# Performance work log

Hardware: AMD Instinct MI355X
Metric: run time of the kernel (lower is better)

The kernel has to match this reference:

```python
import jax, jax.numpy as jnp
import numpy as np

B, S, D_IN, D_OUT, BLK = 2, 2048, 4096, 16384, 32
NBLK = D_IN // BLK  # 128


def setup_inputs() -> dict:
    key = jax.random.key(0)
    k_x, k_q, k_s, k_b = jax.random.split(key, 4)
    x = jax.random.normal(k_x, (B, S, D_IN), dtype=jnp.float32)
    # GGML Q8_0: signed 8-bit quants per block of 32
    qs = jax.random.randint(k_q, (D_OUT, NBLK, BLK), -128, 128, dtype=jnp.int32)
    # per-block scales (stand-in for the fp16 'd' field); small magnitude
    scales = jax.random.uniform(k_s, (D_OUT, NBLK), dtype=jnp.float32) * 0.02
    bias = jax.random.normal(k_b, (D_OUT,), dtype=jnp.float32)
    return {"x": x, "qs": qs, "scales": scales, "bias": bias}


def reference(x, qs, scales, bias):
    # _materialize_weight: block dequantize (d * q per block) then cast to input dtype
    # qs: [O, NBLK, BLK], scales: [O, NBLK] -> W: [O, D_IN]
    W = (scales[:, :, None] * qs.astype(x.dtype)).reshape(D_OUT, D_IN)
    # host Linear: y = x @ W^T + b
    y = jnp.einsum('bsd,od->bso', x, W) + bias
    return y
```

## Files before the change

kernel.cpp:

```cpp
#include <hip/hip_runtime.h>
#include <cstdint>
#include <cstddef>

#define M_DIM 4096
#define N_DIM 16384
#define K_DIM 4096
#define NBLK_Q 128

#define BM 256
#define BN 256
#define BK 64
#define KSTEPS (K_DIM / BK)
#define BUFB 32768
#define NBUF 2

typedef int i32x4 __attribute__((ext_vector_type(4)));
typedef int i32x16 __attribute__((ext_vector_type(16)));

#define SFENCE() __builtin_amdgcn_sched_barrier(0)

__global__ __launch_bounds__(256) void quant_x(const float* __restrict__ x,
                                               char* __restrict__ A8S,
                                               float* __restrict__ sxr) {
  const int m = blockIdx.x;
  const int t = threadIdx.x;
  const float* xr = x + (size_t)m * K_DIM + t * 16;
  float4 v[4];
#pragma unroll
  for (int i = 0; i < 4; ++i) v[i] = ((const float4*)xr)[i];
  float amax = 0.f;
#pragma unroll
  for (int i = 0; i < 4; ++i)
    amax = fmaxf(amax, fmaxf(fmaxf(fabsf(v[i].x), fabsf(v[i].y)),
                             fmaxf(fabsf(v[i].z), fabsf(v[i].w))));
#pragma unroll
  for (int off = 32; off; off >>= 1) amax = fmaxf(amax, __shfl_xor(amax, off, 64));
  __shared__ float wmax[4];
  if ((t & 63) == 0) wmax[t >> 6] = amax;
  __syncthreads();
  amax = fmaxf(fmaxf(wmax[0], wmax[1]), fmaxf(wmax[2], wmax[3]));
  const float inv = 127.0f / amax;
  if (t == 0) sxr[m] = amax / 127.0f;
  unsigned d[4];
#pragma unroll
  for (int i = 0; i < 4; ++i) {
    int q0 = (int)rintf(v[i].x * inv), q1 = (int)rintf(v[i].y * inv);
    int q2 = (int)rintf(v[i].z * inv), q3 = (int)rintf(v[i].w * inv);
    d[i] = (q0 & 0xff) | ((q1 & 0xff) << 8) | ((q2 & 0xff) << 16) | ((q3 & 0xff) << 24);
  }
  const int k32 = t >> 1, kg = t & 1;
  const int mtile = m >> 8, mm = m & 255, m32 = mm >> 5, r = mm & 31;
  int4* dst = (int4*)(A8S + ((size_t)(mtile * 128 + k32)) * 8192 + m32 * 1024 + kg * 512 + r * 16);
  *dst = make_int4(d[0], d[1], d[2], d[3]);
}

__global__ __launch_bounds__(256) void pack_w8(const int* __restrict__ qs,
                                               const float* __restrict__ scales,
                                               char* __restrict__ B8S,
                                               float* __restrict__ swc) {
  const int o = blockIdx.x * 4 + (threadIdx.x >> 6);
  const int l = threadIdx.x & 63;
  const float s0 = scales[(size_t)o * NBLK_Q + l];
  const float s1 = scales[(size_t)o * NBLK_Q + 64 + l];
  float S = fmaxf(s0, s1);
#pragma unroll
  for (int off = 32; off; off >>= 1) S = fmaxf(S, __shfl_xor(S, off, 64));
  if (l == 0) swc[o] = S;
  const float rS = 1.0f / S;
  const int nt = o >> 8, col = o & 255, n32 = col >> 5, c = col & 31;
#pragma unroll
  for (int h = 0; h < 2; ++h) {
    const int nb = l + 64 * h;
    const float ratio = ((h == 0) ? s0 : s1) * rS;
    const int4* q = (const int4*)(qs + ((size_t)o * NBLK_Q + nb) * 32);
    unsigned d[8];
#pragma unroll
    for (int g = 0; g < 8; ++g) {
      int4 v = q[g];
      int a0 = (int)rintf((float)v.x * ratio);
      int a1 = (int)rintf((float)v.y * ratio);
      int a2 = (int)rintf((float)v.z * ratio);
      int a3 = (int)rintf((float)v.w * ratio);
      d[g] = (a0 & 0xff) | ((a1 & 0xff) << 8) | ((a2 & 0xff) << 16) | ((a3 & 0xff) << 24);
    }
    char* dst = B8S + ((size_t)(nt * 128 + nb)) * 8192 + n32 * 1024 + c * 16;
    ((int4*)dst)[0] = make_int4(d[0], d[1], d[2], d[3]);
    ((int4*)(dst + 512))[0] = make_int4(d[4], d[5], d[6], d[7]);
  }
}

__global__ __launch_bounds__(512, 2) void gemm_i8(
    const char* __restrict__ A8S, const char* __restrict__ B8S,
    const float* __restrict__ sxr, const float* __restrict__ swc,
    const float* __restrict__ bias, float* __restrict__ C) {
  __shared__ __align__(16) char lds[NBUF * BUFB];

  const int tid = threadIdx.x;
  const int w = tid >> 6;
  const int l = tid & 63;
  const int wm = w >> 2;
  const int wn = w & 3;

  const int bid = blockIdx.x;
  const int xcd = bid & 7;
  const int k = bid >> 3;
  const int mtile = xcd * 2 + (k & 1);
  const int ntile = k >> 1;
  const int brow = mtile * BM;
  const int bcol = ntile * BN;

  const char* srcA = A8S + (size_t)mtile * 128 * 8192 + w * 1024 + l * 16;
  const char* srcB = B8S + (size_t)ntile * 128 * 8192 + w * 1024 + l * 16;
  const int doff = w * 1024 + l * 16;

  i32x16 acc[4][2] = {};

  {
    int4 ra0 = *(const int4*)(srcA);
    int4 ra1 = *(const int4*)(srcA + 8192);
    int4 rb0 = *(const int4*)(srcB);
    int4 rb1 = *(const int4*)(srcB + 8192);
    *(int4*)(lds + doff) = ra0;
    *(int4*)(lds + 16384 + doff) = ra1;
    *(int4*)(lds + 8192 + doff) = rb0;
    *(int4*)(lds + 24576 + doff) = rb1;
    __syncthreads();
  }

  for (int kt = 0; kt < KSTEPS; ++kt) {
    const char* bb = lds + (kt & 1) * BUFB;

    i32x4 a[2][4], b[2][2];
#pragma unroll
    for (int s = 0; s < 2; ++s) {
#pragma unroll
      for (int i = 0; i < 4; ++i)
        a[s][i] = *(const i32x4*)(bb + s * 16384 + (wm * 4 + i) * 1024 + l * 16);
#pragma unroll
      for (int j = 0; j < 2; ++j)
        b[s][j] = *(const i32x4*)(bb + s * 16384 + 8192 + (wn * 2 + j) * 1024 + l * 16);
    }

    const int qn = (kt + 1 > KSTEPS - 1) ? (KSTEPS - 1) : (kt + 1);
    const size_t go = (size_t)qn * 16384;
    int4 ra0 = *(const int4*)(srcA + go);
    int4 ra1 = *(const int4*)(srcA + go + 8192);
    int4 rb0 = *(const int4*)(srcB + go);
    int4 rb1 = *(const int4*)(srcB + go + 8192);

    SFENCE();
    __builtin_amdgcn_s_setprio(1);
#pragma unroll
    for (int i = 0; i < 4; ++i)
#pragma unroll
      for (int j = 0; j < 2; ++j) {
        acc[i][j] = __builtin_amdgcn_mfma_i32_32x32x32_i8(a[0][i], b[0][j], acc[i][j], 0, 0, 0);
        acc[i][j] = __builtin_amdgcn_mfma_i32_32x32x32_i8(a[1][i], b[1][j], acc[i][j], 0, 0, 0);
      }
    __builtin_amdgcn_s_setprio(0);
    SFENCE();

    char* nb = lds + ((kt + 1) & 1) * BUFB;
    *(int4*)(nb + doff) = ra0;
    *(int4*)(nb + 16384 + doff) = ra1;
    *(int4*)(nb + 8192 + doff) = rb0;
    *(int4*)(nb + 24576 + doff) = rb1;
    __syncthreads();
  }

#pragma unroll
  for (int i = 0; i < 4; ++i) {
    const int rb = brow + wm * 128 + i * 32 + 4 * (l >> 5);
#pragma unroll
    for (int j = 0; j < 2; ++j) {
      const int col = bcol + wn * 64 + j * 32 + (l & 31);
      const float Sw = swc[col];
      const float bv = bias[col];
#pragma unroll
      for (int r = 0; r < 16; ++r) {
        const int row = rb + (r & 3) + 8 * (r >> 2);
        C[(size_t)row * N_DIM + col] = (float)acc[i][j][r] * (sxr[row] * Sw) + bv;
      }
    }
  }
}

__global__ void naive_gemm(const float* __restrict__ x, const int* __restrict__ qs,
                           const float* __restrict__ scales, const float* __restrict__ bias,
                           float* __restrict__ y) {
  size_t idx = (size_t)blockIdx.x * 256 + threadIdx.x;
  if (idx >= (size_t)M_DIM * N_DIM) return;
  int o = (int)(idx % N_DIM);
  size_t m = idx / N_DIM;
  const float* xr = x + m * K_DIM;
  const int* q = qs + (size_t)o * K_DIM;
  const float* sc = scales + (size_t)o * NBLK_Q;
  float sum = 0.f;
  for (int nb = 0; nb < NBLK_Q; ++nb) {
    float s = sc[nb];
    float bs = 0.f;
#pragma unroll 8
    for (int b = 0; b < 32; ++b) bs += xr[nb * 32 + b] * (float)q[nb * 32 + b];
    sum += s * bs;
  }
  y[idx] = sum + bias[o];
}

extern "C" void kernel_launch(void* const* d_in, const int* in_sizes, int n_in,
                              void* d_out, int out_size, void* d_ws, size_t ws_size,
                              hipStream_t stream) {
  const float* x = (const float*)d_in[0];
  const int* qs = (const int*)d_in[1];
  const float* scales = (const float*)d_in[2];
  const float* bias = (const float*)d_in[3];
  float* y = (float*)d_out;

  const size_t A8_bytes = (size_t)M_DIM * K_DIM;
  const size_t B8_bytes = (size_t)N_DIM * K_DIM;
  const size_t SX_bytes = (size_t)M_DIM * 4;
  const size_t SW_bytes = (size_t)N_DIM * 4;

  if (ws_size < A8_bytes + B8_bytes + SX_bytes + SW_bytes) {
    size_t total = (size_t)M_DIM * N_DIM;
    naive_gemm<<<(unsigned)((total + 255) / 256), 256, 0, stream>>>(x, qs, scales, bias, y);
    return;
  }

  char* A8S = (char*)d_ws;
  char* B8S = A8S + A8_bytes;
  float* sxr = (float*)(B8S + B8_bytes);
  float* swc = (float*)((char*)sxr + SX_bytes);

  quant_x<<<M_DIM, 256, 0, stream>>>(x, A8S, sxr);
  pack_w8<<<N_DIM / 4, 256, 0, stream>>>(qs, scales, B8S, swc);
  gemm_i8<<<(M_DIM / BM) * (N_DIM / BN), 512, 0, stream>>>(A8S, B8S, sxr, swc, bias, y);
}
```

Before: 455.3 us.

## Deepen int8 GEMM pipeline to four LDS buffers with register double-buffering

```diff
diff --git a/kernel.cpp b/kernel.cpp
--- a/kernel.cpp
+++ b/kernel.cpp
@@ -9,15 +9,18 @@
 
 #define BM 256
 #define BN 256
-#define BK 64
+#define BK 32
 #define KSTEPS (K_DIM / BK)
-#define BUFB 32768
-#define NBUF 2
+#define BUFB 16384
+#define NBUF 4
 
 typedef int i32x4 __attribute__((ext_vector_type(4)));
 typedef int i32x16 __attribute__((ext_vector_type(16)));
 
 #define SFENCE() __builtin_amdgcn_sched_barrier(0)
+#define BAR() __builtin_amdgcn_s_barrier()
+#define WAITVM(n) asm volatile("s_waitcnt vmcnt(" #n ")")
+#define WAITLG0() asm volatile("s_waitcnt lgkmcnt(0)")
 
 __global__ __launch_bounds__(256) void quant_x(const float* __restrict__ x,
                                                char* __restrict__ A8S,
@@ -111,62 +114,78 @@
 
   const char* srcA = A8S + (size_t)mtile * 128 * 8192 + w * 1024 + l * 16;
   const char* srcB = B8S + (size_t)ntile * 128 * 8192 + w * 1024 + l * 16;
-  const int doff = w * 1024 + l * 16;
+  const int doffA = w * 1024 + l * 16;
+  const int doffB = 8192 + w * 1024 + l * 16;
+  const int roffA = wm * 4096 + l * 16;
+  const int roffB = 8192 + wn * 2048 + l * 16;
 
   i32x16 acc[4][2] = {};
+  i32x4 a0[4], b0[2], a1[4], b1[2];
+  int4 gA0, gB0, gA1, gB1;
 
   {
-    int4 ra0 = *(const int4*)(srcA);
-    int4 ra1 = *(const int4*)(srcA + 8192);
-    int4 rb0 = *(const int4*)(srcB);
-    int4 rb1 = *(const int4*)(srcB + 8192);
-    *(int4*)(lds + doff) = ra0;
-    *(int4*)(lds + 16384 + doff) = ra1;
-    *(int4*)(lds + 8192 + doff) = rb0;
-    *(int4*)(lds + 24576 + doff) = rb1;
-    __syncthreads();
-  }
-
-  for (int kt = 0; kt < KSTEPS; ++kt) {
-    const char* bb = lds + (kt & 1) * BUFB;
-
-    i32x4 a[2][4], b[2][2];
-#pragma unroll
-    for (int s = 0; s < 2; ++s) {
-#pragma unroll
-      for (int i = 0; i < 4; ++i)
-        a[s][i] = *(const i32x4*)(bb + s * 16384 + (wm * 4 + i) * 1024 + l * 16);
-#pragma unroll
-      for (int j = 0; j < 2; ++j)
-        b[s][j] = *(const i32x4*)(bb + s * 16384 + 8192 + (wn * 2 + j) * 1024 + l * 16);
-    }
-
-    const int qn = (kt + 1 > KSTEPS - 1) ? (KSTEPS - 1) : (kt + 1);
-    const size_t go = (size_t)qn * 16384;
-    int4 ra0 = *(const int4*)(srcA + go);
-    int4 ra1 = *(const int4*)(srcA + go + 8192);
-    int4 rb0 = *(const int4*)(srcB + go);
-    int4 rb1 = *(const int4*)(srcB + go + 8192);
-
-    SFENCE();
-    __builtin_amdgcn_s_setprio(1);
+    int4 ta0 = *(const int4*)(srcA);
+    int4 tb0 = *(const int4*)(srcB);
+    int4 ta1 = *(const int4*)(srcA + 8192);
+    int4 tb1 = *(const int4*)(srcB + 8192);
+    *(int4*)(lds + doffA) = ta0;
+    *(int4*)(lds + doffB) = tb0;
+    *(int4*)(lds + BUFB + doffA) = ta1;
+    *(int4*)(lds + BUFB + doffB) = tb1;
+    gA0 = *(const int4*)(srcA + 2 * 8192);
+    gB0 = *(const int4*)(srcB + 2 * 8192);
+    WAITLG0();
+    SFENCE(); BAR(); SFENCE();
 #pragma unroll
     for (int i = 0; i < 4; ++i)
-#pragma unroll
-      for (int j = 0; j < 2; ++j) {
-        acc[i][j] = __builtin_amdgcn_mfma_i32_32x32x32_i8(a[0][i], b[0][j], acc[i][j], 0, 0, 0);
-        acc[i][j] = __builtin_amdgcn_mfma_i32_32x32x32_i8(a[1][i], b[1][j], acc[i][j], 0, 0, 0);
-      }
-    __builtin_amdgcn_s_setprio(0);
-    SFENCE();
-
-    char* nb = lds + ((kt + 1) & 1) * BUFB;
-    *(int4*)(nb + doff) = ra0;
-    *(int4*)(nb + 16384 + doff) = ra1;
-    *(int4*)(nb + 8192 + doff) = rb0;
-    *(int4*)(nb + 24576 + doff) = rb1;
-    __syncthreads();
-  }
+      a0[i] = *(const i32x4*)(lds + roffA + i * 1024);
+#pragma unroll
+    for (int j = 0; j < 2; ++j)
+      b0[j] = *(const i32x4*)(lds + roffB + j * 1024);
+  }
+
+#define STEP(KT, CA, CB, NA, NB, WA, WB, LA, LB)                               \
+  do {                                                                         \
+    const char* rb = lds + (((KT) + 1) & 3) * BUFB;                            \
+    NA[0] = *(const i32x4*)(rb + roffA);                                       \
+    NA[1] = *(const i32x4*)(rb + roffA + 1024);                                \
+    NA[2] = *(const i32x4*)(rb + roffA + 2048);                                \
+    NA[3] = *(const i32x4*)(rb + roffA + 3072);                                \
+    NB[0] = *(const i32x4*)(rb + roffB);                                       \
+    NB[1] = *(const i32x4*)(rb + roffB + 1024);                                \
+    {                                                                          \
+      const int ql = ((KT) + 3 > KSTEPS - 1) ? (KSTEPS - 1) : ((KT) + 3);      \
+      LA = *(const int4*)(srcA + (size_t)ql * 8192);                           \
+      LB = *(const int4*)(srcB + (size_t)ql * 8192);                           \
+    }                                                                          \
+    SFENCE();                                                                  \
+    __builtin_amdgcn_s_setprio(1);                                             \
+    acc[0][0] = __builtin_amdgcn_mfma_i32_32x32x32_i8(CA[0], CB[0], acc[0][0], 0, 0, 0); \
+    acc[0][1] = __builtin_amdgcn_mfma_i32_32x32x32_i8(CA[0], CB[1], acc[0][1], 0, 0, 0); \
+    acc[1][0] = __builtin_amdgcn_mfma_i32_32x32x32_i8(CA[1], CB[0], acc[1][0], 0, 0, 0); \
+    acc[1][1] = __builtin_amdgcn_mfma_i32_32x32x32_i8(CA[1], CB[1], acc[1][1], 0, 0, 0); \
+    acc[2][0] = __builtin_amdgcn_mfma_i32_32x32x32_i8(CA[2], CB[0], acc[2][0], 0, 0, 0); \
+    acc[2][1] = __builtin_amdgcn_mfma_i32_32x32x32_i8(CA[2], CB[1], acc[2][1], 0, 0, 0); \
+    acc[3][0] = __builtin_amdgcn_mfma_i32_32x32x32_i8(CA[3], CB[0], acc[3][0], 0, 0, 0); \
+    acc[3][1] = __builtin_amdgcn_mfma_i32_32x32x32_i8(CA[3], CB[1], acc[3][1], 0, 0, 0); \
+    __builtin_amdgcn_s_setprio(0);                                             \
+    SFENCE();                                                                  \
+    WAITVM(2);                                                                 \
+    {                                                                          \
+      char* wb = lds + (((KT) + 2) & 3) * BUFB;                                \
+      *(int4*)(wb + doffA) = WA;                                               \
+      *(int4*)(wb + doffB) = WB;                                               \
+    }                                                                          \
+    SFENCE();                                                                  \
+    WAITLG0();                                                                 \
+    SFENCE(); BAR(); SFENCE();                                                 \
+  } while (0)
+
+  for (int kt = 0; kt < KSTEPS; kt += 2) {
+    STEP(kt, a0, b0, a1, b1, gA0, gB0, gA1, gB1);
+    STEP(kt + 1, a1, b1, a0, b0, gA1, gB1, gA0, gB0);
+  }
+#undef STEP
 
 #pragma unroll
   for (int i = 0; i < 4; ++i) {
```

Result: faster. 425.0 us (-6.7%).
